# Kernel optimization log

Measured on AMD Instinct MI355X. Metric: run time of the kernel, lower is better.

## Reference

```python
import jax, jax.numpy as jnp
import numpy as np

# iRPE config: ratio=1.9, method='euc', mode='ctx', shared_head=True, skip=1, rpe_on='k'
ALPHA, BETA, GAMMA = 1.9, 3.8, 15.2  # alpha=1*ratio, beta=2*ratio, gamma=8*ratio
NUM_HEADS = 12


def _rp_bucket_euc(height, width, skip):
    """Static relative-position bucket ids (Euclidean method, piecewise index).
    Returns (skip+L, skip+L) int array and num_buckets."""
    coords = np.stack(np.meshgrid(np.arange(height), np.arange(width), indexing='ij'), -1)
    coords = coords.reshape(-1, 2).astype(np.float64)  # (L, 2)
    diff = coords[:, None, :] - coords[None, :, :]      # (L, L, 2)
    dis = np.round(np.sqrt((diff ** 2).sum(-1)))        # (L, L), nonnegative
    # piecewise_index: identity for dis<=alpha, log-spaced (rounded, clipped at beta) beyond
    log_idx = np.minimum(
        np.round(ALPHA + np.log(np.maximum(dis, 1e-9) / ALPHA) / np.log(GAMMA / ALPHA) * (BETA - ALPHA)),
        BETA).astype(np.int64)
    bucket = np.where(dis <= ALPHA, np.round(dis).astype(np.int64), log_idx)
    bucket = bucket - bucket.min()
    nb = 2 * int(BETA) + 1  # 7
    if skip > 0:
        L = height * width
        full = np.full((skip + L, skip + L), nb, dtype=np.int64)  # extra bucket for cls token
        full[skip:, skip:] = bucket
        bucket, nb = full, nb + 1  # nb = 8
    return jnp.asarray(bucket), nb


def setup_inputs() -> dict:
    key = jax.random.key(0)
    ks = jax.random.split(key, 4)
    B, N, C = 8, 1025, 768  # 32x32 patches + 1 cls token
    hd = C // NUM_HEADS
    nb = 2 * int(BETA) + 1 + 1  # 8 buckets (incl. skip bucket)
    return {
        "x": jax.random.normal(ks[0], (B, N, C), jnp.float32),
        "qkv_w": jax.random.normal(ks[1], (3 * C, C), jnp.float32) * 0.02,
        "proj_w": jax.random.normal(ks[2], (C, C), jnp.float32) * 0.02,
        "proj_b": jnp.zeros((C,), jnp.float32),
        "rpe_w": jax.random.normal(ks[3], (hd, nb), jnp.float32) * 0.02,  # shared across heads
    }


def reference(x, qkv_w, proj_w, proj_b, rpe_w):
    B, N, C = x.shape
    H = NUM_HEADS
    hd = C // H
    scale = hd ** -0.5
    n_modalities = 1
    height = int((N // n_modalities) ** 0.5)        # 32 (mask is None path)
    skip = N - n_modalities * height * height       # 1 (cls token)
    rp_bucket, _ = _rp_bucket_euc(height, height, skip)  # (N, N) int, static

    qkv = (x @ qkv_w.T).reshape(B, N, 3, H, hd).transpose(2, 0, 3, 1, 4)  # (3,B,H,N,hd)
    q, k, v = qkv[0] * scale, qkv[1], qkv[2]
    attn = jnp.einsum('bhid,bhjd->bhij', q, k)
    # contextual RPE on keys (shared head): bias[b,h,i,j] = q[b,h,i,:] @ rpe_w[:, bucket[i,j]]
    lookup = jnp.einsum('bhid,dm->bhim', q, rpe_w)                      # (B,H,N,nb)
    bias = jnp.take_along_axis(lookup, rp_bucket[None, None, :, :], axis=3)  # (B,H,N,N)
    attn = jax.nn.softmax(attn + bias, axis=-1)
    out = jnp.einsum('bhij,bhjd->bhid', attn, v)
    out = out.transpose(0, 2, 1, 3).reshape(B, N, C)
    return out @ proj_w.T + proj_b
```

## Files before the change

### kernel.cpp

```cpp
#include <hip/hip_runtime.h>
#include <math.h>

#define B_    8
#define N_    1025
#define H_    12
#define HD_   64
#define C_    768
#define BH_   (B_*H_)
#define NTOK  (B_*N_)
#define SCALE 0.125f
#define NPAD  1092
#define NPADV 1088

#define QKV_ELEMS (BH_*N_*HD_)

#define XB_OFF_B     ((size_t)0)
#define WQKV_OFF_B   (XB_OFF_B + (size_t)NTOK*C_*2)
#define WPROJ_OFF_B  (WQKV_OFF_B + (size_t)3*C_*C_*2)
#define QB_OFF_B     (WPROJ_OFF_B + (size_t)C_*C_*2)
#define KB_OFF_B     (QB_OFF_B + (size_t)QKV_ELEMS*2)
#define AOB_OFF_B    (KB_OFF_B + (size_t)QKV_ELEMS*2)
#define VT_OFF_B     (AOB_OFF_B + (size_t)QKV_ELEMS*2)
#define BUCKET_OFF_B (VT_OFF_B + (size_t)BH_*HD_*NPADV*2)

typedef __attribute__((ext_vector_type(8))) short s8bf;
typedef __attribute__((ext_vector_type(8))) unsigned short u8s;
typedef __attribute__((ext_vector_type(4))) float v4f;
typedef unsigned short ushort_t;

#define GLOAD16(gp, lp) __builtin_amdgcn_global_load_lds( \
    (const __attribute__((address_space(1))) unsigned int*)(gp), \
    (__attribute__((address_space(3))) unsigned int*)(lp), 16, 0, 0)

#define SBAR() do { \
    __builtin_amdgcn_sched_barrier(0); \
    asm volatile("s_barrier" ::: "memory"); \
    __builtin_amdgcn_sched_barrier(0); \
} while (0)

__device__ __forceinline__ unsigned short f2bf(float x) {
    union { float f; unsigned u; } v; v.f = x;
    unsigned r = v.u + 0x7FFFu + ((v.u >> 16) & 1u);
    return (unsigned short)(r >> 16);
}

__global__ void bucket_kernel(unsigned char* __restrict__ bucketT) {
    int tid = blockIdx.x * 256 + threadIdx.x;
    if (tid >= N_ * NPAD) return;
    unsigned ut = (unsigned)tid;
    int j = ut / (unsigned)NPAD, i = ut % (unsigned)NPAD;
    if (i >= N_) i = N_ - 1;
    int bk;
    if (i < 1 || j < 1) {
        bk = 7;
    } else {
        int pi = i - 1, pj = j - 1;
        int dy = (pi >> 5) - (pj >> 5);
        int dx = (pi & 31) - (pj & 31);
        int d2 = dy*dy + dx*dx;
        bk = (d2 == 0) ? 0 : ((d2 <= 2) ? 1 : ((d2 <= 12) ? 2 : 3));
    }
    bucketT[tid] = (unsigned char)bk;
}

__global__ __launch_bounds__(256) void cast_kernel(
        const float* __restrict__ x, const float* __restrict__ w1,
        const float* __restrict__ w2,
        ushort_t* __restrict__ xb, ushort_t* __restrict__ w1b,
        ushort_t* __restrict__ w2b) {
    const int NX = NTOK * C_ / 8, NW1 = 3 * C_ * C_ / 8, NW2 = C_ * C_ / 8;
    int g = blockIdx.x * 256 + threadIdx.x;
    const float* src; ushort_t* dst; int idx;
    if (g < NX)                 { src = x;  dst = xb;  idx = g; }
    else if (g < NX + NW1)      { src = w1; dst = w1b; idx = g - NX; }
    else if (g < NX + NW1 + NW2){ src = w2; dst = w2b; idx = g - NX - NW1; }
    else return;
    size_t off = (size_t)idx * 8;
    float4 a = *(const float4*)(src + off);
    float4 c = *(const float4*)(src + off + 4);
    __align__(16) ushort_t h[8] = {f2bf(a.x), f2bf(a.y), f2bf(a.z), f2bf(a.w),
                                   f2bf(c.x), f2bf(c.y), f2bf(c.z), f2bf(c.w)};
    *(u8s*)(dst + off) = *(u8s*)h;
}

__global__ __launch_bounds__(256) void qkv_kernel(
        const ushort_t* __restrict__ xb, const ushort_t* __restrict__ wb,
        ushort_t* __restrict__ qb, ushort_t* __restrict__ kb, ushort_t* __restrict__ vt) {
    __shared__ __align__(16) ushort_t As0[128*64];
    __shared__ __align__(16) ushort_t Bs0[128*64];
    __shared__ __align__(16) ushort_t As1[128*64];
    __shared__ __align__(16) ushort_t Bs1[128*64];
    const int L = blockIdx.x + blockIdx.y * 65;
    const int xcd = L & 7, idx = L >> 3;
    const int wg = (xcd < 2 ? xcd * 147 : 2 * 147 + (xcd - 2) * 146) + idx;
    const int m0 = (wg / 18) * 128, c0 = (wg % 18) * 128;
    const int t = threadIdx.x;
    const int w = t >> 6, lane = t & 63, lc = lane & 15, lq = lane >> 4;
    const int wm = (w >> 1) * 64, wn = (w & 1) * 64;
    const int srow8 = w * 32 + (lane >> 3);
    const int gsw8  = (((lane & 7) ^ (lane >> 3)) & 7) * 8;

    v4f acc[4][4];
#pragma unroll
    for (int mt = 0; mt < 4; mt++)
#pragma unroll
        for (int nt = 0; nt < 4; nt++) acc[mt][nt] = (v4f){0.f, 0.f, 0.f, 0.f};

    auto STAGE = [&](ushort_t* Ad, ushort_t* Bd, int k0) {
#pragma unroll
        for (int i = 0; i < 4; i++) {
            int row = srow8 + i * 8;
            int m = m0 + row; if (m > NTOK - 1) m = NTOK - 1;
            GLOAD16(xb + (size_t)m * C_ + k0 + gsw8,           &Ad[(w*32 + i*8) * 64]);
            GLOAD16(wb + (size_t)(c0 + row) * C_ + k0 + gsw8,  &Bd[(w*32 + i*8) * 64]);
        }
    };
    auto COMPUTE = [&](const ushort_t* A, const ushort_t* B) {
#pragma unroll
        for (int kk = 0; kk < 64; kk += 32) {
            s8bf af[4], bf[4];
#pragma unroll
            for (int mt = 0; mt < 4; mt++)
                af[mt] = *(const s8bf*)&A[(wm + mt*16 + lc) * 64 + ((((kk>>3) + lq) ^ (lc & 7)) * 8)];
#pragma unroll
            for (int nt = 0; nt < 4; nt++)
                bf[nt] = *(const s8bf*)&B[(wn + nt*16 + lc) * 64 + ((((kk>>3) + lq) ^ (lc & 7)) * 8)];
#pragma unroll
            for (int mt = 0; mt < 4; mt++)
#pragma unroll
                for (int nt = 0; nt < 4; nt++)
                    acc[mt][nt] = __builtin_amdgcn_mfma_f32_16x16x32_bf16(af[mt], bf[nt], acc[mt][nt], 0, 0, 0);
        }
    };

    STAGE(As0, Bs0, 0);
#pragma unroll
    for (int it = 0; it < 6; ++it) {
        const int k0 = it * 128;
        if (k0 + 64 < C_) {
            STAGE(As1, Bs1, k0 + 64);
            asm volatile("s_waitcnt vmcnt(8)" ::: "memory");
        } else {
            asm volatile("s_waitcnt vmcnt(0)" ::: "memory");
        }
        SBAR();
        COMPUTE(As0, Bs0);
        SBAR();
        if (k0 + 128 < C_) {
            STAGE(As0, Bs0, k0 + 128);
            asm volatile("s_waitcnt vmcnt(8)" ::: "memory");
        } else {
            asm volatile("s_waitcnt vmcnt(0)" ::: "memory");
        }
        SBAR();
        COMPUTE(As1, Bs1);
        if (it < 5) SBAR();
    }

#pragma unroll
    for (int mt = 0; mt < 4; mt++) {
#pragma unroll
        for (int r = 0; r < 4; r++) {
            int m = m0 + wm + mt*16 + lq*4 + r;
            if (m >= NTOK) continue;
            unsigned um = (unsigned)m;
            int b = um / (unsigned)N_, n = um % (unsigned)N_;
#pragma unroll
            for (int nt = 0; nt < 4; nt++) {
                int c = c0 + wn + nt*16 + lc;
                int comp = c / C_, rem = c % C_;
                int h = rem >> 6, d0 = rem & 63;
                float val = acc[mt][nt][r] * ((comp == 0) ? SCALE : 1.0f);
                if (comp == 2) {
                    vt[((size_t)((b*H_ + h)*HD_ + d0))*NPADV + n] = f2bf(val);
                } else {
                    ushort_t* dst = (comp == 0) ? qb : kb;
                    dst[((size_t)((b*H_ + h)*N_ + n))*HD_ + d0] = f2bf(val);
                }
            }
        }
    }
}

#define LDT  72
#define LUTS 9

__global__ __launch_bounds__(256) void attn_kernel(
        const ushort_t* __restrict__ qb, const ushort_t* __restrict__ kb,
        const ushort_t* __restrict__ vt, const float* __restrict__ rpe,
        const unsigned char* __restrict__ bucketT, ushort_t* __restrict__ ao) {
    __shared__ __align__(16) ushort_t Ks[64*LDT];
    __shared__ __align__(16) ushort_t Vs[64*LDT];
    __shared__ float lut[64*LUTS];

    const int bh = blockIdx.x, it = blockIdx.y;
    const int b  = bh / H_, hh = bh % H_;
    const int i0 = it * 64;
    const int t  = threadIdx.x;
    const int w  = t >> 6, lane = t & 63, lc = lane & 15, lq = lane >> 4;
    const int row_w = w * 16;

    const ushort_t* qp = qb + (size_t)bh * N_ * HD_;
    const ushort_t* kp = kb + (size_t)bh * N_ * HD_;
    const ushort_t* vp = vt + (size_t)bh * HD_ * NPADV;

    {
        int row = t >> 2, d0 = (t & 3) * 16;
        int gi = i0 + row;
        u8s h0 = (u8s)0, h1 = (u8s)0;
        if (gi < N_) {
            h0 = *(const u8s*)(qp + (size_t)gi * HD_ + d0);
            h1 = *(const u8s*)(qp + (size_t)gi * HD_ + d0 + 8);
        }
        *(u8s*)&Vs[row*LDT + d0]     = h0;
        *(u8s*)&Vs[row*LDT + d0 + 8] = h1;
    }
    if (t < 64) {
        float4 r0 = *(const float4*)(rpe + t*8);
        float4 r1 = *(const float4*)(rpe + t*8 + 4);
        Ks[0*LDT + t] = f2bf(r0.x); Ks[1*LDT + t] = f2bf(r0.y);
        Ks[2*LDT + t] = f2bf(r0.z); Ks[3*LDT + t] = f2bf(r0.w);
        Ks[4*LDT + t] = f2bf(r1.x); Ks[5*LDT + t] = f2bf(r1.y);
        Ks[6*LDT + t] = f2bf(r1.z); Ks[7*LDT + t] = f2bf(r1.w);
    } else if (t < 128) {
        int idx = t - 64;
        int m = 8 + (idx >> 3), c = (idx & 7) * 8;
        *(u8s*)&Ks[m*LDT + c] = (u8s)0;
    }
    __syncthreads();

    s8bf qf0 = *(s8bf*)&Vs[(row_w + lc)*LDT + lq*8];
    s8bf qf1 = *(s8bf*)&Vs[(row_w + lc)*LDT + 32 + lq*8];

    {
        s8bf rf0 = *(s8bf*)&Ks[lc*LDT + lq*8];
        s8bf rf1 = *(s8bf*)&Ks[lc*LDT + 32 + lq*8];
        v4f la = (v4f){0.f, 0.f, 0.f, 0.f};
        la = __builtin_amdgcn_mfma_f32_16x16x32_bf16(qf0, rf0, la, 0, 0, 0);
        la = __builtin_amdgcn_mfma_f32_16x16x32_bf16(qf1, rf1, la, 0, 0, 0);
        if (lc < 8) {
#pragma unroll
            for (int r = 0; r < 4; r++)
                lut[(row_w + lq*4 + r)*LUTS + lc] = la[r];
        }
    }

    const int srow = t >> 2, sd0 = (t & 3) * 16;
    const int kslot = ((srow >> 5) * 2 + ((srow >> 2) & 1)) * 16 + ((srow >> 3) & 3) * 4 + (srow & 3);
    u8s krg0, krg1, vrg0, vrg1;
    {
        const ushort_t* ks = kp + (size_t)srow * HD_ + sd0;
        krg0 = *(const u8s*)ks; krg1 = *(const u8s*)(ks + 8);
        const ushort_t* vs = vp + (size_t)srow * NPADV + sd0;
        vrg0 = *(const u8s*)vs; vrg1 = *(const u8s*)(vs + 8);
    }
    int myrow = i0 + row_w + lc; if (myrow > N_ - 1) myrow = N_ - 1;
    const unsigned char* bkrow = bucketT + (size_t)myrow * NPAD;
    const int lutbase = (row_w + lc) * LUTS;
    const int jb0 = 8*lq, jb1 = 8*lq + 4, jb2 = 8*lq + 32, jb3 = 8*lq + 36;
    unsigned bk4[4];
    bk4[0] = *(const unsigned*)(bkrow + jb0);
    bk4[1] = *(const unsigned*)(bkrow + jb1);
    bk4[2] = *(const unsigned*)(bkrow + jb2);
    bk4[3] = *(const unsigned*)(bkrow + jb3);

    v4f o[4];
    float lsum = 0.f;
#pragma unroll
    for (int dt = 0; dt < 4; dt++) o[dt] = (v4f){0.f, 0.f, 0.f, 0.f};

    for (int jt = 0; jt < 17; jt++) {
        const int j0 = jt * 64;
        __syncthreads();
        {
            ushort_t* kd = &Ks[kslot*LDT + sd0];
            *(u8s*)kd = krg0; *(u8s*)(kd + 8) = krg1;
            ushort_t* vd = &Vs[srow*LDT + sd0];
            *(u8s*)vd = vrg0; *(u8s*)(vd + 8) = vrg1;
        }
        __syncthreads();

        unsigned bk4n[4];
        if (jt < 16) {
            int gj = j0 + 64 + srow; if (gj > N_ - 1) gj = N_ - 1;
            const ushort_t* ks = kp + (size_t)gj * HD_ + sd0;
            krg0 = *(const u8s*)ks; krg1 = *(const u8s*)(ks + 8);
            const ushort_t* vs = vp + (size_t)srow * NPADV + (j0 + 64) + sd0;
            vrg0 = *(const u8s*)vs; vrg1 = *(const u8s*)(vs + 8);
            bk4n[0] = *(const unsigned*)(bkrow + j0 + 64 + jb0);
            bk4n[1] = *(const unsigned*)(bkrow + j0 + 64 + jb1);
            bk4n[2] = *(const unsigned*)(bkrow + j0 + 64 + jb2);
            bk4n[3] = *(const unsigned*)(bkrow + j0 + 64 + jb3);
        }

        v4f acc[4];
#pragma unroll
        for (int t4 = 0; t4 < 4; t4++) acc[t4] = (v4f){0.f, 0.f, 0.f, 0.f};
#pragma unroll
        for (int t4 = 0; t4 < 4; t4++) {
            s8bf kf0 = *(s8bf*)&Ks[(t4*16 + lc)*LDT + lq*8];
            s8bf kf1 = *(s8bf*)&Ks[(t4*16 + lc)*LDT + 32 + lq*8];
            acc[t4] = __builtin_amdgcn_mfma_f32_16x16x32_bf16(kf0, qf0, acc[t4], 0, 0, 0);
            acc[t4] = __builtin_amdgcn_mfma_f32_16x16x32_bf16(kf1, qf1, acc[t4], 0, 0, 0);
        }

        float pp[4][4];
        const int jbs[4] = {jb0, jb1, jb2, jb3};
#pragma unroll
        for (int t4 = 0; t4 < 4; t4++) {
#pragma unroll
            for (int r = 0; r < 4; r++) {
                int bk = (bk4[t4] >> (8*r)) & 0xFF;
                float sv = acc[t4][r] + lut[lutbase + bk];
                float p = __expf(sv);
                if (jt == 16 && (jbs[t4] + r) > 0) p = 0.f;
                lsum += p;
                pp[t4][r] = p;
            }
        }
#pragma unroll
        for (int t4 = 0; t4 < 4; t4++) bk4[t4] = bk4n[t4];

        __align__(16) ushort_t ph[16] = {
            f2bf(pp[0][0]), f2bf(pp[0][1]), f2bf(pp[0][2]), f2bf(pp[0][3]),
            f2bf(pp[1][0]), f2bf(pp[1][1]), f2bf(pp[1][2]), f2bf(pp[1][3]),
            f2bf(pp[2][0]), f2bf(pp[2][1]), f2bf(pp[2][2]), f2bf(pp[2][3]),
            f2bf(pp[3][0]), f2bf(pp[3][1]), f2bf(pp[3][2]), f2bf(pp[3][3])};
        s8bf pf0 = *(s8bf*)&ph[0];
        s8bf pf1 = *(s8bf*)&ph[8];

#pragma unroll
        for (int dt = 0; dt < 4; dt++) {
            s8bf vf0 = *(s8bf*)&Vs[(dt*16 + lc)*LDT + lq*8];
            s8bf vf1 = *(s8bf*)&Vs[(dt*16 + lc)*LDT + 32 + lq*8];
            o[dt] = __builtin_amdgcn_mfma_f32_16x16x32_bf16(pf0, vf0, o[dt], 0, 0, 0);
            o[dt] = __builtin_amdgcn_mfma_f32_16x16x32_bf16(pf1, vf1, o[dt], 0, 0, 0);
        }
    }

    lsum += __shfl_xor(lsum, 16);
    lsum += __shfl_xor(lsum, 32);
    if (lq == 0) lut[(row_w + lc)*LUTS + 8] = lsum;
    __builtin_amdgcn_s_waitcnt(0);
#pragma unroll
    for (int r = 0; r < 4; r++) {
        int i = i0 + row_w + lq*4 + r;
        if (i < N_) {
            float inv = 1.0f / lut[(row_w + lq*4 + r)*LUTS + 8];
#pragma unroll
            for (int dt = 0; dt < 4; dt++)
                ao[((size_t)(b*N_ + i))*C_ + hh*HD_ + dt*16 + lc] = f2bf(o[dt][r] * inv);
        }
    }
}

__global__ __launch_bounds__(256) void proj_kernel(
        const ushort_t* __restrict__ ab, const ushort_t* __restrict__ wb,
        const float* __restrict__ bias, float* __restrict__ out) {
    __shared__ __align__(16) ushort_t As0[128*64];
    __shared__ __align__(16) ushort_t Bs0[128*64];
    __shared__ __align__(16) ushort_t As1[128*64];
    __shared__ __align__(16) ushort_t Bs1[128*64];
    const int L = blockIdx.x + blockIdx.y * 65;
    const int xcd = L & 7, idx = L >> 3;
    const int wg = (xcd < 6 ? xcd * 49 : 6 * 49 + (xcd - 6) * 48) + idx;
    const int m0 = (wg / 6) * 128, c0 = (wg % 6) * 128;
    const int t = threadIdx.x;
    const int w = t >> 6, lane = t & 63, lc = lane & 15, lq = lane >> 4;
    const int wm = (w >> 1) * 64, wn = (w & 1) * 64;
    const int srow8 = w * 32 + (lane >> 3);
    const int gsw8  = (((lane & 7) ^ (lane >> 3)) & 7) * 8;

    v4f acc[4][4];
#pragma unroll
    for (int mt = 0; mt < 4; mt++)
#pragma unroll
        for (int nt = 0; nt < 4; nt++) acc[mt][nt] = (v4f){0.f, 0.f, 0.f, 0.f};

    auto STAGE = [&](ushort_t* Ad, ushort_t* Bd, int k0) {
#pragma unroll
        for (int i = 0; i < 4; i++) {
            int row = srow8 + i * 8;
            int m = m0 + row; if (m > NTOK - 1) m = NTOK - 1;
            GLOAD16(ab + (size_t)m * C_ + k0 + gsw8,           &Ad[(w*32 + i*8) * 64]);
            GLOAD16(wb + (size_t)(c0 + row) * C_ + k0 + gsw8,  &Bd[(w*32 + i*8) * 64]);
        }
    };
    auto COMPUTE = [&](const ushort_t* A, const ushort_t* B) {
#pragma unroll
        for (int kk = 0; kk < 64; kk += 32) {
            s8bf af[4], bf[4];
#pragma unroll
            for (int mt = 0; mt < 4; mt++)
                af[mt] = *(const s8bf*)&A[(wm + mt*16 + lc) * 64 + ((((kk>>3) + lq) ^ (lc & 7)) * 8)];
#pragma unroll
            for (int nt = 0; nt < 4; nt++)
                bf[nt] = *(const s8bf*)&B[(wn + nt*16 + lc) * 64 + ((((kk>>3) + lq) ^ (lc & 7)) * 8)];
#pragma unroll
            for (int mt = 0; mt < 4; mt++)
#pragma unroll
                for (int nt = 0; nt < 4; nt++)
                    acc[mt][nt] = __builtin_amdgcn_mfma_f32_16x16x32_bf16(af[mt], bf[nt], acc[mt][nt], 0, 0, 0);
        }
    };

    STAGE(As0, Bs0, 0);
#pragma unroll
    for (int it = 0; it < 6; ++it) {
        const int k0 = it * 128;
        if (k0 + 64 < C_) {
            STAGE(As1, Bs1, k0 + 64);
            asm volatile("s_waitcnt vmcnt(8)" ::: "memory");
        } else {
            asm volatile("s_waitcnt vmcnt(0)" ::: "memory");
        }
        SBAR();
        COMPUTE(As0, Bs0);
        SBAR();
        if (k0 + 128 < C_) {
            STAGE(As0, Bs0, k0 + 128);
            asm volatile("s_waitcnt vmcnt(8)" ::: "memory");
        } else {
            asm volatile("s_waitcnt vmcnt(0)" ::: "memory");
        }
        SBAR();
        COMPUTE(As1, Bs1);
        if (it < 5) SBAR();
    }

    float pb[4];
#pragma unroll
    for (int nt = 0; nt < 4; nt++) pb[nt] = bias[c0 + wn + nt*16 + lc];
#pragma unroll
    for (int mt = 0; mt < 4; mt++) {
#pragma unroll
        for (int r = 0; r < 4; r++) {
            int m = m0 + wm + mt*16 + lq*4 + r;
            if (m >= NTOK) continue;
#pragma unroll
            for (int nt = 0; nt < 4; nt++) {
                int c = c0 + wn + nt*16 + lc;
                out[(size_t)m * C_ + c] = acc[mt][nt][r] + pb[nt];
            }
        }
    }
}

extern "C" void kernel_launch(void* const* d_in, const int* in_sizes, int n_in,
                              void* d_out, int out_size, void* d_ws, size_t ws_size,
                              hipStream_t stream) {
    const float* x      = (const float*)d_in[0];
    const float* qkv_w  = (const float*)d_in[1];
    const float* proj_w = (const float*)d_in[2];
    const float* proj_b = (const float*)d_in[3];
    const float* rpe_w  = (const float*)d_in[4];
    float* out = (float*)d_out;

    char* ws = (char*)d_ws;
    ushort_t* xb   = (ushort_t*)(ws + XB_OFF_B);
    ushort_t* wqkv = (ushort_t*)(ws + WQKV_OFF_B);
    ushort_t* wprj = (ushort_t*)(ws + WPROJ_OFF_B);
    ushort_t* qb   = (ushort_t*)(ws + QB_OFF_B);
    ushort_t* kb   = (ushort_t*)(ws + KB_OFF_B);
    ushort_t* aob  = (ushort_t*)(ws + AOB_OFF_B);
    ushort_t* vt   = (ushort_t*)(ws + VT_OFF_B);
    unsigned char* bucketT = (unsigned char*)(ws + BUCKET_OFF_B);

    const int ncast = (NTOK*C_ + 3*C_*C_ + C_*C_) / 8;
    bucket_kernel<<<dim3((N_*NPAD + 255)/256), 256, 0, stream>>>(bucketT);
    cast_kernel<<<dim3((ncast + 255)/256), 256, 0, stream>>>(x, qkv_w, proj_w, xb, wqkv, wprj);
    qkv_kernel<<<dim3(65, 18), 256, 0, stream>>>(xb, wqkv, qb, kb, vt);
    attn_kernel<<<dim3(96, 17), 256, 0, stream>>>(qb, kb, vt, rpe_w, bucketT, aob);
    proj_kernel<<<dim3(65, 6), 256, 0, stream>>>(aob, wprj, proj_b, out);
}
```

Before: 231.1 us.

## Swizzle LDS tiles, peel last key tile, pack bf16 probabilities pairwise

```diff
diff --git a/kernel.cpp b/kernel.cpp
--- a/kernel.cpp
+++ b/kernel.cpp
@@ -42,6 +42,10 @@
     union { float f; unsigned u; } v; v.f = x;
     unsigned r = v.u + 0x7FFFu + ((v.u >> 16) & 1u);
     return (unsigned short)(r >> 16);
+}
+__device__ __forceinline__ unsigned packbf_hu(float lo, float hi) {
+    union { float f; unsigned u; } a, b; a.f = lo; b.f = hi;
+    return ((a.u + 0x8000u) >> 16) | ((b.u + 0x8000u) & 0xFFFF0000u);
 }
 
 __global__ void bucket_kernel(unsigned char* __restrict__ bucketT) {
@@ -182,15 +186,14 @@
     }
 }
 
-#define LDT  72
 #define LUTS 9
 
 __global__ __launch_bounds__(256) void attn_kernel(
         const ushort_t* __restrict__ qb, const ushort_t* __restrict__ kb,
         const ushort_t* __restrict__ vt, const float* __restrict__ rpe,
         const unsigned char* __restrict__ bucketT, ushort_t* __restrict__ ao) {
-    __shared__ __align__(16) ushort_t Ks[64*LDT];
-    __shared__ __align__(16) ushort_t Vs[64*LDT];
+    __shared__ __align__(16) ushort_t Ks[64*64];
+    __shared__ __align__(16) ushort_t Vs[64*64];
     __shared__ float lut[64*LUTS];
 
     const int bh = blockIdx.x, it = blockIdx.y;
@@ -199,42 +202,46 @@
     const int t  = threadIdx.x;
     const int w  = t >> 6, lane = t & 63, lc = lane & 15, lq = lane >> 4;
     const int row_w = w * 16;
+    const int rs = lc & 7;
+    const int gA = ((lq ^ rs) & 7) * 8;
+    const int gB = (((lq + 4) ^ rs) & 7) * 8;
 
     const ushort_t* qp = qb + (size_t)bh * N_ * HD_;
     const ushort_t* kp = kb + (size_t)bh * N_ * HD_;
     const ushort_t* vp = vt + (size_t)bh * HD_ * NPADV;
 
     {
-        int row = t >> 2, d0 = (t & 3) * 16;
+        int row = t >> 2, g0 = (t & 3) * 2, qrs = row & 7;
         int gi = i0 + row;
         u8s h0 = (u8s)0, h1 = (u8s)0;
         if (gi < N_) {
-            h0 = *(const u8s*)(qp + (size_t)gi * HD_ + d0);
-            h1 = *(const u8s*)(qp + (size_t)gi * HD_ + d0 + 8);
-        }
-        *(u8s*)&Vs[row*LDT + d0]     = h0;
-        *(u8s*)&Vs[row*LDT + d0 + 8] = h1;
+            h0 = *(const u8s*)(qp + (size_t)gi * HD_ + g0*8);
+            h1 = *(const u8s*)(qp + (size_t)gi * HD_ + g0*8 + 8);
+        }
+        *(u8s*)&Vs[row*64 + ((g0 ^ qrs) * 8)]       = h0;
+        *(u8s*)&Vs[row*64 + (((g0+1) ^ qrs) * 8)]   = h1;
     }
     if (t < 64) {
         float4 r0 = *(const float4*)(rpe + t*8);
         float4 r1 = *(const float4*)(rpe + t*8 + 4);
-        Ks[0*LDT + t] = f2bf(r0.x); Ks[1*LDT + t] = f2bf(r0.y);
-        Ks[2*LDT + t] = f2bf(r0.z); Ks[3*LDT + t] = f2bf(r0.w);
-        Ks[4*LDT + t] = f2bf(r1.x); Ks[5*LDT + t] = f2bf(r1.y);
-        Ks[6*LDT + t] = f2bf(r1.z); Ks[7*LDT + t] = f2bf(r1.w);
+        const int gr = t >> 3, go = t & 7;
+        float vals[8] = {r0.x, r0.y, r0.z, r0.w, r1.x, r1.y, r1.z, r1.w};
+#pragma unroll
+        for (int m = 0; m < 8; m++)
+            Ks[m*64 + ((gr ^ (m & 7)) * 8) + go] = f2bf(vals[m]);
     } else if (t < 128) {
         int idx = t - 64;
-        int m = 8 + (idx >> 3), c = (idx & 7) * 8;
-        *(u8s*)&Ks[m*LDT + c] = (u8s)0;
+        int m = 8 + (idx >> 3), g = idx & 7;
+        *(u8s*)&Ks[m*64 + ((g ^ (m & 7)) * 8)] = (u8s)0;
     }
     __syncthreads();
 
-    s8bf qf0 = *(s8bf*)&Vs[(row_w + lc)*LDT + lq*8];
-    s8bf qf1 = *(s8bf*)&Vs[(row_w + lc)*LDT + 32 + lq*8];
+    s8bf qf0 = *(s8bf*)&Vs[(row_w + lc)*64 + gA];
+    s8bf qf1 = *(s8bf*)&Vs[(row_w + lc)*64 + gB];
 
     {
-        s8bf rf0 = *(s8bf*)&Ks[lc*LDT + lq*8];
-        s8bf rf1 = *(s8bf*)&Ks[lc*LDT + 32 + lq*8];
+        s8bf rf0 = *(s8bf*)&Ks[lc*64 + gA];
+        s8bf rf1 = *(s8bf*)&Ks[lc*64 + gB];
         v4f la = (v4f){0.f, 0.f, 0.f, 0.f};
         la = __builtin_amdgcn_mfma_f32_16x16x32_bf16(qf0, rf0, la, 0, 0, 0);
         la = __builtin_amdgcn_mfma_f32_16x16x32_bf16(qf1, rf1, la, 0, 0, 0);
@@ -245,8 +252,13 @@
         }
     }
 
-    const int srow = t >> 2, sd0 = (t & 3) * 16;
+    const int srow = t >> 2, g0 = (t & 3) * 2, sd0 = g0 * 8;
     const int kslot = ((srow >> 5) * 2 + ((srow >> 2) & 1)) * 16 + ((srow >> 3) & 3) * 4 + (srow & 3);
+    const int krs = kslot & 7, vrs = srow & 7;
+    ushort_t* const kd0 = &Ks[kslot*64 + ((g0 ^ krs) * 8)];
+    ushort_t* const kd1 = &Ks[kslot*64 + (((g0+1) ^ krs) * 8)];
+    ushort_t* const vd0 = &Vs[srow*64 + ((g0 ^ vrs) * 8)];
+    ushort_t* const vd1 = &Vs[srow*64 + (((g0+1) ^ vrs) * 8)];
     u8s krg0, krg1, vrg0, vrg1;
     {
         const ushort_t* ks = kp + (size_t)srow * HD_ + sd0;
@@ -269,19 +281,17 @@
 #pragma unroll
     for (int dt = 0; dt < 4; dt++) o[dt] = (v4f){0.f, 0.f, 0.f, 0.f};
 
-    for (int jt = 0; jt < 17; jt++) {
+    for (int jt = 0; jt < 16; jt++) {
         const int j0 = jt * 64;
         __syncthreads();
         {
-            ushort_t* kd = &Ks[kslot*LDT + sd0];
-            *(u8s*)kd = krg0; *(u8s*)(kd + 8) = krg1;
-            ushort_t* vd = &Vs[srow*LDT + sd0];
-            *(u8s*)vd = vrg0; *(u8s*)(vd + 8) = vrg1;
+            *(u8s*)kd0 = krg0; *(u8s*)kd1 = krg1;
+            *(u8s*)vd0 = vrg0; *(u8s*)vd1 = vrg1;
         }
         __syncthreads();
 
         unsigned bk4n[4];
-        if (jt < 16) {
+        {
             int gj = j0 + 64 + srow; if (gj > N_ - 1) gj = N_ - 1;
             const ushort_t* ks = kp + (size_t)gj * HD_ + sd0;
             krg0 = *(const u8s*)ks; krg1 = *(const u8s*)(ks + 8);
@@ -298,41 +308,81 @@
         for (int t4 = 0; t4 < 4; t4++) acc[t4] = (v4f){0.f, 0.f, 0.f, 0.f};
 #pragma unroll
         for (int t4 = 0; t4 < 4; t4++) {
-            s8bf kf0 = *(s8bf*)&Ks[(t4*16 + lc)*LDT + lq*8];
-            s8bf kf1 = *(s8bf*)&Ks[(t4*16 + lc)*LDT + 32 + lq*8];
+            s8bf kf0 = *(s8bf*)&Ks[(t4*16 + lc)*64 + gA];
+            s8bf kf1 = *(s8bf*)&Ks[(t4*16 + lc)*64 + gB];
             acc[t4] = __builtin_amdgcn_mfma_f32_16x16x32_bf16(kf0, qf0, acc[t4], 0, 0, 0);
             acc[t4] = __builtin_amdgcn_mfma_f32_16x16x32_bf16(kf1, qf1, acc[t4], 0, 0, 0);
         }
 
-        float pp[4][4];
+        unsigned pw[8];
+#pragma unroll
+        for (int t4 = 0; t4 < 4; t4++) {
+            float p0, p1, p2, p3;
+            {
+                int k0b = (bk4[t4]      ) & 0xFF; p0 = __expf(acc[t4][0] + lut[lutbase + k0b]);
+                int k1b = (bk4[t4] >>  8) & 0xFF; p1 = __expf(acc[t4][1] + lut[lutbase + k1b]);
+                int k2b = (bk4[t4] >> 16) & 0xFF; p2 = __expf(acc[t4][2] + lut[lutbase + k2b]);
+                int k3b = (bk4[t4] >> 24)       ; p3 = __expf(acc[t4][3] + lut[lutbase + k3b]);
+            }
+            lsum += (p0 + p1) + (p2 + p3);
+            pw[t4*2]     = packbf_hu(p0, p1);
+            pw[t4*2 + 1] = packbf_hu(p2, p3);
+        }
+#pragma unroll
+        for (int t4 = 0; t4 < 4; t4++) bk4[t4] = bk4n[t4];
+        s8bf pf0 = *(s8bf*)&pw[0];
+        s8bf pf1 = *(s8bf*)&pw[4];
+
+#pragma unroll
+        for (int dt = 0; dt < 4; dt++) {
+            s8bf vf0 = *(s8bf*)&Vs[(dt*16 + lc)*64 + gA];
+            s8bf vf1 = *(s8bf*)&Vs[(dt*16 + lc)*64 + gB];
+            o[dt] = __builtin_amdgcn_mfma_f32_16x16x32_bf16(pf0, vf0, o[dt], 0, 0, 0);
+            o[dt] = __builtin_amdgcn_mfma_f32_16x16x32_bf16(pf1, vf1, o[dt], 0, 0, 0);
+        }
+    }
+
+    {
+        __syncthreads();
+        {
+            *(u8s*)kd0 = krg0; *(u8s*)kd1 = krg1;
+            *(u8s*)vd0 = vrg0; *(u8s*)vd1 = vrg1;
+        }
+        __syncthreads();
+
+        v4f acc[4];
+#pragma unroll
+        for (int t4 = 0; t4 < 4; t4++) acc[t4] = (v4f){0.f, 0.f, 0.f, 0.f};
+#pragma unroll
+        for (int t4 = 0; t4 < 4; t4++) {
+            s8bf kf0 = *(s8bf*)&Ks[(t4*16 + lc)*64 + gA];
+            s8bf kf1 = *(s8bf*)&Ks[(t4*16 + lc)*64 + gB];
+            acc[t4] = __builtin_amdgcn_mfma_f32_16x16x32_bf16(kf0, qf0, acc[t4], 0, 0, 0);
+            acc[t4] = __builtin_amdgcn_mfma_f32_16x16x32_bf16(kf1, qf1, acc[t4], 0, 0, 0);
+        }
+
+        unsigned pw[8];
         const int jbs[4] = {jb0, jb1, jb2, jb3};
 #pragma unroll
         for (int t4 = 0; t4 < 4; t4++) {
+            float pv[4];
 #pragma unroll
             for (int r = 0; r < 4; r++) {
                 int bk = (bk4[t4] >> (8*r)) & 0xFF;
-                float sv = acc[t4][r] + lut[lutbase + bk];
-                float p = __expf(sv);
-                if (jt == 16 && (jbs[t4] + r) > 0) p = 0.f;
+                float p = __expf(acc[t4][r] + lut[lutbase + bk]);
+                if ((jbs[t4] + r) > 0) p = 0.f;
                 lsum += p;
-                pp[t4][r] = p;
+                pv[r] = p;
             }
-        }
-#pragma unroll
-        for (int t4 = 0; t4 < 4; t4++) bk4[t4] = bk4n[t4];
-
-        __align__(16) ushort_t ph[16] = {
-            f2bf(pp[0][0]), f2bf(pp[0][1]), f2bf(pp[0][2]), f2bf(pp[0][3]),
-            f2bf(pp[1][0]), f2bf(pp[1][1]), f2bf(pp[1][2]), f2bf(pp[1][3]),
-            f2bf(pp[2][0]), f2bf(pp[2][1]), f2bf(pp[2][2]), f2bf(pp[2][3]),
-            f2bf(pp[3][0]), f2bf(pp[3][1]), f2bf(pp[3][2]), f2bf(pp[3][3])};
-        s8bf pf0 = *(s8bf*)&ph[0];
-        s8bf pf1 = *(s8bf*)&ph[8];
-
+            pw[t4*2]     = packbf_hu(pv[0], pv[1]);
+            pw[t4*2 + 1] = packbf_hu(pv[2], pv[3]);
+        }
+        s8bf pf0 = *(s8bf*)&pw[0];
+        s8bf pf1 = *(s8bf*)&pw[4];
 #pragma unroll
         for (int dt = 0; dt < 4; dt++) {
-            s8bf vf0 = *(s8bf*)&Vs[(dt*16 + lc)*LDT + lq*8];
-            s8bf vf1 = *(s8bf*)&Vs[(dt*16 + lc)*LDT + 32 + lq*8];
+            s8bf vf0 = *(s8bf*)&Vs[(dt*16 + lc)*64 + gA];
+            s8bf vf1 = *(s8bf*)&Vs[(dt*16 + lc)*64 + gB];
             o[dt] = __builtin_amdgcn_mfma_f32_16x16x32_bf16(pf0, vf0, o[dt], 0, 0, 0);
             o[dt] = __builtin_amdgcn_mfma_f32_16x16x32_bf16(pf1, vf1, o[dt], 0, 0, 0);
         }
```

New measurement: 225.5 us. 1.03x faster.
